# Kernel tuning notes

Hardware: AMD Instinct MI355X
Metric: run time of the kernel (lower is better)

The kernel has to match this reference:

```python
import jax, jax.numpy as jnp
import numpy as np

N, S, K, D, H = 65536, 5, 4, 12, 48  # batch, sq_len, max_node_num, nodefeat_n1, lstm hidden


def setup_inputs() -> dict:
    key = jax.random.key(0)
    ks = jax.random.split(key, 32)
    f = lambda i, shape, s=0.1: jax.random.normal(ks[i], shape, dtype=jnp.float32) * s
    return {
        'nodes_feature': f(0, (N, S, K, 6), 1.0),
        'pos': f(1, (N, S, K, 6), 1.0),
        'attmat': jax.random.uniform(ks[2], (N, S, K, K), dtype=jnp.float32),
        'msg_w': f(3, (D, D)), 'msg_b': f(4, (D,)),
        'gru_w_ih': f(5, (3 * D, D)), 'gru_w_hh': f(6, (3 * D, D)),
        'gru_b_ih': f(7, (3 * D,)), 'gru_b_hh': f(8, (3 * D,)),
        'lstm_w_ih_fw': f(9, (4 * H, H)), 'lstm_w_hh_fw': f(10, (4 * H, H)),
        'lstm_b_ih_fw': f(11, (4 * H,)), 'lstm_b_hh_fw': f(12, (4 * H,)),
        'lstm_w_ih_bw': f(13, (4 * H, H)), 'lstm_w_hh_bw': f(14, (4 * H, H)),
        'lstm_b_ih_bw': f(15, (4 * H,)), 'lstm_b_hh_bw': f(16, (4 * H,)),
        'en1_w': f(17, (H, 2 * H)), 'en1_b': f(18, (H,)),
        'en2_w': f(19, (36, H)), 'en2_b': f(20, (36,)),
        'en3_w': f(21, (6, 36)), 'en3_b': f(22, (6,)),
    }


def _gru_cell(x, h, w_ih, w_hh, b_ih, b_hh):
    # torch.nn.GRU single step: gates ordered r, z, n
    gi = x @ w_ih.T + b_ih
    gh = h @ w_hh.T + b_hh
    ir, iz, inn = jnp.split(gi, 3, axis=-1)
    hr, hz, hn = jnp.split(gh, 3, axis=-1)
    r = jax.nn.sigmoid(ir + hr)
    z = jax.nn.sigmoid(iz + hz)
    n = jnp.tanh(inn + r * hn)
    return (1.0 - z) * n + z * h


def _lstm_dir(x, w_ih, w_hh, b_ih, b_hh):
    # x: [T, N, H]; torch.nn.LSTM gates ordered i, f, g, o. Returns final hidden [N, H].
    nb = x.shape[1]
    hh = w_hh.shape[1]
    def step(carry, xt):
        h, c = carry
        g = xt @ w_ih.T + b_ih + h @ w_hh.T + b_hh
        i, fg, gg, o = jnp.split(g, 4, axis=-1)
        c = jax.nn.sigmoid(fg) * c + jax.nn.sigmoid(i) * jnp.tanh(gg)
        h = jax.nn.sigmoid(o) * jnp.tanh(c)
        return (h, c), None
    init = (jnp.zeros((nb, hh), x.dtype), jnp.zeros((nb, hh), x.dtype))
    (h, _), _ = jax.lax.scan(step, init, x)
    return h


def reference(nodes_feature, pos, attmat, msg_w, msg_b,
              gru_w_ih, gru_w_hh, gru_b_ih, gru_b_hh,
              lstm_w_ih_fw, lstm_w_hh_fw, lstm_b_ih_fw, lstm_b_hh_fw,
              lstm_w_ih_bw, lstm_w_hh_bw, lstm_b_ih_bw, lstm_b_hh_bw,
              en1_w, en1_b, en2_w, en2_b, en3_w, en3_b):
    node_feat = jnp.concatenate([nodes_feature, pos], axis=-1)  # [N,S,K,12]

    def message_pass(h):
        # message_fun on all neighbor states, attention-weighted sum, GRU update.
        m_all = h @ msg_w.T + msg_b                       # [N,S,K,12]
        m_v = jnp.einsum('bsnw,bswd->bsnd', attmat, m_all)  # [N,S,K,12]
        return _gru_cell(m_v, h, gru_w_ih, gru_w_hh, gru_b_ih, gru_b_hh)

    h = message_pass(node_feat)  # pass 0 (reads node_feat for h_v and h_w)
    h = message_pass(h)          # pass 1 (reads pass-0 hidden state)

    # hidden_node_state is stored [..., feat, node]; view(5,-1) flattens (feat, node)
    x = jnp.transpose(h, (0, 1, 3, 2)).reshape(h.shape[0], S, D * K)  # [N,S,48]
    xt = jnp.transpose(x, (1, 0, 2))  # [S,N,48]
    h_fw = _lstm_dir(xt, lstm_w_ih_fw, lstm_w_hh_fw, lstm_b_ih_fw, lstm_b_hh_fw)
    h_bw = _lstm_dir(xt[::-1], lstm_w_ih_bw, lstm_w_hh_bw, lstm_b_ih_bw, lstm_b_hh_bw)
    hn = jnp.concatenate([h_fw, h_bw], axis=-1)  # [N,96] == h_n.view(-1) per batch

    e = jax.nn.relu(hn @ en1_w.T + en1_b)
    e = jax.nn.relu(e @ en2_w.T + en2_b)
    return e @ en3_w.T + en3_b  # pred_label [N,6]
```

## Files before the change

kernel.cpp:

```cpp
#include <hip/hip_runtime.h>
#include <cstddef>

#define NB 65536
#define SL 5

typedef _Float16 f16;
typedef f16 half8 __attribute__((ext_vector_type(8)));
typedef float f32x4 __attribute__((ext_vector_type(4)));

__device__ __forceinline__ float sigm(float x) {
  return __builtin_amdgcn_rcpf(1.0f + __expf(-x));
}
__device__ __forceinline__ float tanh_f(float x) {
  return __builtin_fmaf(2.0f, __builtin_amdgcn_rcpf(1.0f + __expf(-2.0f * x)), -1.0f);
}
__device__ __forceinline__ unsigned int pkh2(float a, float b) {
  return (unsigned int)__builtin_bit_cast(unsigned short, (_Float16)a)
       | ((unsigned int)__builtin_bit_cast(unsigned short, (_Float16)b) << 16);
}
__device__ __forceinline__ unsigned int pku2(unsigned short a, unsigned short b) {
  return (unsigned int)a | ((unsigned int)b << 16);
}
__device__ __forceinline__ float loh(unsigned int u) {
  return (float)__builtin_bit_cast(_Float16, (unsigned short)(u & 0xffffu));
}
__device__ __forceinline__ float hih(unsigned int u) {
  return (float)__builtin_bit_cast(_Float16, (unsigned short)(u >> 16));
}

__global__ __launch_bounds__(256) void prep_kernel(
    const float* __restrict__ wi_fw, const float* __restrict__ wh_fw,
    const float* __restrict__ bi_fw, const float* __restrict__ bh_fw,
    const float* __restrict__ wi_bw, const float* __restrict__ wh_bw,
    const float* __restrict__ bi_bw, const float* __restrict__ bh_bw,
    const float* __restrict__ msg_w, const float* __restrict__ msg_b,
    const float* __restrict__ gw_ih, const float* __restrict__ gw_hh,
    const float* __restrict__ gb_ih, const float* __restrict__ gb_hh,
    unsigned short* __restrict__ wfrag, float* __restrict__ bsum,
    unsigned short* __restrict__ mfrag, float* __restrict__ mbias)
{
  const int t = blockIdx.x * 256 + threadIdx.x;
  if (t < 36864) {
    const int i = t & 7, lane = (t >> 3) & 63, fid = t >> 9;
    const int kc = fid % 3, mt = (fid / 3) % 3, ug = (fid / 9) & 3, dir = fid / 36;
    const int k = kc * 32 + (lane >> 4) * 8 + i;
    const int r16 = lane & 15;
    const int j = ug * 12 + mt * 4 + (r16 >> 2);
    const int g = r16 & 3;
    const float* wi = dir ? wi_bw : wi_fw;
    const float* wh = dir ? wh_bw : wh_fw;
    const float v = (k < 48) ? wi[(g * 48 + j) * 48 + k] : wh[(g * 48 + j) * 48 + (k - 48)];
    wfrag[t] = __builtin_bit_cast(unsigned short, (_Float16)v);
  } else if (t < 37248) {
    const int q = t - 36864;
    const int r16 = q & 15, mt = (q >> 4) % 3, ug = (q / 48) & 3, dir = q / 192;
    const int j = ug * 12 + mt * 4 + (r16 >> 2);
    const int g = r16 & 3;
    const int row = g * 48 + j;
    bsum[q] = dir ? (bi_bw[row] + bh_bw[row]) : (bi_fw[row] + bh_fw[row]);
  } else if (t < 39296) {
    const int q = t - 37248;
    const int i = q & 7, lane = (q >> 3) & 63, fid = q >> 9;
    const int k = ((lane >> 4) << 3) + i;
    const int r16 = lane & 15;
    float v = 0.0f;
    if (fid == 0) {
      if (r16 < 12 && k >= 12 && k < 24) v = msg_w[r16 * 12 + (k - 12)];
    } else {
      const int R = (fid - 1) * 16 + r16;
      const int kind = R / 12, j = R % 12;
      if (kind == 0)      v = (k < 12) ? gw_ih[j * 12 + k]          : ((k < 24) ? gw_hh[j * 12 + (k - 12)] : 0.0f);
      else if (kind == 1) v = (k < 12) ? gw_ih[(12 + j) * 12 + k]   : ((k < 24) ? gw_hh[(12 + j) * 12 + (k - 12)] : 0.0f);
      else if (kind == 2) v = (k < 12) ? gw_ih[(24 + j) * 12 + k]   : 0.0f;
      else                v = (k >= 12 && k < 24) ? gw_hh[(24 + j) * 12 + (k - 12)] : 0.0f;
    }
    mfrag[q] = __builtin_bit_cast(unsigned short, (_Float16)v);
  } else if (t < 39360) {
    const int q = t - 39296;
    if (q < 16) mbias[q] = (q < 12) ? msg_b[q] : 0.0f;
    else {
      const int R = q - 16, kind = R / 12, j = R % 12;
      float v;
      if (kind == 0)      v = gb_ih[j] + gb_hh[j];
      else if (kind == 1) v = gb_ih[12 + j] + gb_hh[12 + j];
      else if (kind == 2) v = gb_ih[24 + j];
      else                v = gb_hh[24 + j];
      mbias[q] = v;
    }
  }
}

__global__ __launch_bounds__(256) void msg_mfma_kernel(
    const float* __restrict__ nf, const float* __restrict__ pos,
    const float* __restrict__ att,
    const unsigned short* __restrict__ mfrag, const float* __restrict__ mbias,
    unsigned short* __restrict__ xth)
{
  __shared__ unsigned short B_lds[256][40];
  __shared__ unsigned short g_lds[256][50];
  unsigned short* xbuf = &g_lds[0][0];

  const int tid  = threadIdx.x;
  const int lane = tid & 63;
  const int w    = __builtin_amdgcn_readfirstlane(tid >> 6);
  const int c16  = lane & 15;
  const int grp  = lane >> 4;
  const int own  = tid;
  const int node = own & 3;
  const int sl   = (own >> 6) * 16 + ((own >> 4) & 3) * 4 + ((own >> 2) & 3);

  half8 A1 = *reinterpret_cast<const half8*>(mfrag + (size_t)lane * 8);
  half8 A2[3];
#pragma unroll
  for (int mt = 0; mt < 3; ++mt)
    A2[mt] = *reinterpret_cast<const half8*>(mfrag + (size_t)((1 + mt) * 64 + lane) * 8);
  const f32x4 bias1 = *reinterpret_cast<const f32x4*>(mbias + grp * 4);
  f32x4 bias2[3];
#pragma unroll
  for (int mt = 0; mt < 3; ++mt)
    bias2[mt] = *reinterpret_cast<const f32x4*>(mbias + 16 + mt * 16 + grp * 4);

  {
    unsigned int* bz = reinterpret_cast<unsigned int*>(&B_lds[0][0]);
#pragma unroll
    for (int q = 0; q < 6; ++q)  bz[tid * 20 + q] = 0u;
#pragma unroll
    for (int q = 12; q < 16; ++q) bz[tid * 20 + q] = 0u;
  }

  const int sid = blockIdx.x * 64 + sl;
  const int s   = sid >> 16;
  const int b   = sid & (NB - 1);
  float h[12];
  {
    const size_t ib = ((size_t)(b * SL + s) * 4 + node) * 6;
    const float2* n2 = (const float2*)(nf  + ib);
    const float2* p2 = (const float2*)(pos + ib);
#pragma unroll
    for (int q = 0; q < 3; q++) {
      float2 v = n2[q]; h[q*2]   = v.x; h[q*2+1]   = v.y;
      float2 u = p2[q]; h[6+q*2] = u.x; h[6+q*2+1] = u.y;
    }
  }
  float ta[4];
  {
    float4 v = *(const float4*)(att + ((size_t)(b * SL + s) * 4 + node) * 4);
    ta[0] = v.x; ta[1] = v.y; ta[2] = v.z; ta[3] = v.w;
  }
  {
    unsigned int* bp = (unsigned int*)&B_lds[own][0];
#pragma unroll
    for (int d = 0; d < 6; ++d) bp[6 + d] = pkh2(h[2*d], h[2*d+1]);
  }
  __syncthreads();

#pragma unroll 1
  for (int pass = 0; pass < 2; ++pass) {
#pragma unroll
    for (int nt = 0; nt < 4; ++nt) {
      const int col = w * 64 + nt * 16 + c16;
      half8 B = *reinterpret_cast<const half8*>(&B_lds[col][grp * 8]);
      f32x4 C = __builtin_amdgcn_mfma_f32_16x16x32_f16(A1, B, bias1, 0, 0, 0);
      if (grp < 3) {
        unsigned int* gp = (unsigned int*)&g_lds[col][0];
        gp[grp * 2]     = pkh2(C[0], C[1]);
        gp[grp * 2 + 1] = pkh2(C[2], C[3]);
      }
    }
    __syncthreads();

    {
      const int cb = own & ~3;
      float mv[12];
#pragma unroll
      for (int d = 0; d < 12; ++d) mv[d] = 0.0f;
#pragma unroll
      for (int ww = 0; ww < 4; ++ww) {
        const float a = ta[ww];
        const unsigned int* gp = (const unsigned int*)&g_lds[cb + ww][0];
#pragma unroll
        for (int dq = 0; dq < 6; ++dq) {
          const unsigned int u = gp[dq];
          mv[2*dq]   = __builtin_fmaf(a, loh(u), mv[2*dq]);
          mv[2*dq+1] = __builtin_fmaf(a, hih(u), mv[2*dq+1]);
        }
      }
      unsigned int* bp = (unsigned int*)&B_lds[own][0];
#pragma unroll
      for (int d = 0; d < 6; ++d) bp[d] = pkh2(mv[2*d], mv[2*d+1]);
    }
    __syncthreads();

#pragma unroll
    for (int nt = 0; nt < 4; ++nt) {
      const int col = w * 64 + nt * 16 + c16;
      half8 B = *reinterpret_cast<const half8*>(&B_lds[col][grp * 8]);
      f32x4 C0 = __builtin_amdgcn_mfma_f32_16x16x32_f16(A2[0], B, bias2[0], 0, 0, 0);
      f32x4 C1 = __builtin_amdgcn_mfma_f32_16x16x32_f16(A2[1], B, bias2[1], 0, 0, 0);
      f32x4 C2 = __builtin_amdgcn_mfma_f32_16x16x32_f16(A2[2], B, bias2[2], 0, 0, 0);
      unsigned int* gp = (unsigned int*)&g_lds[col][0];
      gp[grp * 2]      = pkh2(C0[0], C0[1]);
      gp[grp * 2 + 1]  = pkh2(C0[2], C0[3]);
      gp[8 + grp * 2]     = pkh2(C1[0], C1[1]);
      gp[8 + grp * 2 + 1] = pkh2(C1[2], C1[3]);
      gp[16 + grp * 2]     = pkh2(C2[0], C2[1]);
      gp[16 + grp * 2 + 1] = pkh2(C2[2], C2[3]);
    }
    __syncthreads();

    {
      unsigned int ur[6], uz[6], ui[6], uh[6];
      const unsigned int* gq = (const unsigned int*)&g_lds[own][0];
#pragma unroll
      for (int jq = 0; jq < 6; ++jq) {
        ur[jq] = gq[jq];
        uz[jq] = gq[6 + jq];
        ui[jq] = gq[12 + jq];
        uh[jq] = gq[18 + jq];
      }
      if (pass) __syncthreads();
#pragma unroll
      for (int jq = 0; jq < 6; ++jq) {
        {
          const float r = sigm(loh(ur[jq])), z = sigm(loh(uz[jq]));
          const float g = tanh_f(loh(ui[jq]) + r * loh(uh[jq]));
          h[2*jq] = (1.0f - z) * g + z * h[2*jq];
        }
        {
          const float r = sigm(hih(ur[jq])), z = sigm(hih(uz[jq]));
          const float g = tanh_f(hih(ui[jq]) + r * hih(uh[jq]));
          h[2*jq+1] = (1.0f - z) * g + z * h[2*jq+1];
        }
      }
      if (pass == 0) {
        unsigned int* bp = (unsigned int*)&B_lds[own][0];
#pragma unroll
        for (int d = 0; d < 6; ++d) bp[6 + d] = pkh2(h[2*d], h[2*d+1]);
      } else {
#pragma unroll
        for (int d = 0; d < 12; ++d)
          xbuf[sl * 50 + d * 4 + node] =
              __builtin_bit_cast(unsigned short, (_Float16)h[d]);
      }
    }
    __syncthreads();
  }

  const int b0   = (blockIdx.x * 64) & (NB - 1);
  const int sblk = blockIdx.x >> 10;
#pragma unroll
  for (int ff = 0; ff < 12; ++ff) {
    const int f = w * 12 + ff;
    xth[(size_t)(sblk * 48 + f) * NB + b0 + lane] = xbuf[lane * 50 + f];
  }
}

__global__ __launch_bounds__(512) void lstm_mfma_kernel(
    const unsigned short* __restrict__ xth,
    const unsigned short* __restrict__ wfrag,
    const float* __restrict__ bsum,
    const float* __restrict__ e1w, const float* __restrict__ e1b,
    const float* __restrict__ e2w, const float* __restrict__ e2b,
    const float* __restrict__ e3w, const float* __restrict__ e3b,
    float* __restrict__ out)
{
  __shared__ __align__(16) unsigned char poolc[33536];
  unsigned short* act = (unsigned short*)poolc;
  float*          hf  = (float*)poolc;
  unsigned short* e1o = (unsigned short*)(poolc + 26624);
  float*          e2o = (float*)poolc;

  const int tid  = threadIdx.x;
  const int lane = tid & 63;
  const int w    = __builtin_amdgcn_readfirstlane(tid >> 6);
  const int dir  = w & 1;
  const int ug   = w >> 1;
  const int b0   = blockIdx.x * 64;
  const int col  = lane & 15;
  const int grp  = lane >> 4;

  half8 A[3][3];
#pragma unroll
  for (int mt = 0; mt < 3; ++mt)
#pragma unroll
    for (int kc = 0; kc < 3; ++kc) {
      const int fid = ((dir * 4 + ug) * 3 + mt) * 3 + kc;
      A[mt][kc] = *reinterpret_cast<const half8*>(wfrag + (size_t)(fid * 64 + lane) * 8);
    }
  unsigned int bp[3][2];
#pragma unroll
  for (int mt = 0; mt < 3; ++mt) {
    const f32x4 bf = *reinterpret_cast<const f32x4*>(bsum + ((dir * 4 + ug) * 3 + mt) * 16 + grp * 4);
    bp[mt][0] = pkh2(bf[0], bf[1]);
    bp[mt][1] = pkh2(bf[2], bf[3]);
  }

  {
    unsigned short xa[6], xb[6];
#pragma unroll
    for (int ff = 0; ff < 6; ++ff) {
      const int f = w * 6 + ff;
      xa[ff] = xth[(size_t)(0 * 48 + f) * NB + b0 + lane];
      xb[ff] = xth[(size_t)(4 * 48 + f) * NB + b0 + lane];
    }
    unsigned int* a0 = (unsigned int*)&act[(0 * 64 + lane) * 104 + w * 6];
    unsigned int* a1 = (unsigned int*)&act[(1 * 64 + lane) * 104 + w * 6];
#pragma unroll
    for (int u = 0; u < 3; ++u) {
      a0[u] = pku2(xa[2*u], xa[2*u+1]);
      a1[u] = pku2(xb[2*u], xb[2*u+1]);
    }
  }
#pragma unroll
  for (int jj = 0; jj < 6; ++jj)
    *(unsigned int*)&act[(dir * 64 + lane) * 104 + 48 + ug * 12 + jj * 2] = 0u;
  __syncthreads();

  float c[3][4];
#pragma unroll
  for (int mt = 0; mt < 3; ++mt)
#pragma unroll
    for (int nt = 0; nt < 4; ++nt) c[mt][nt] = 0.0f;

#pragma unroll 1
  for (int st = 0; st < 5; ++st) {
    unsigned int hp[3][2];
#pragma unroll
    for (int nt = 0; nt < 4; ++nt) {
      const int n = nt * 16 + col;
      const unsigned short* ar = &act[(dir * 64 + n) * 104];
      half8 B0 = *reinterpret_cast<const half8*>(ar + grp * 8);
      half8 B1 = *reinterpret_cast<const half8*>(ar + 32 + grp * 8);
      half8 B2 = *reinterpret_cast<const half8*>(ar + 64 + grp * 8);
      f32x4 C0, C1, C2;
      C0[0] = loh(bp[0][0]); C0[1] = hih(bp[0][0]); C0[2] = loh(bp[0][1]); C0[3] = hih(bp[0][1]);
      C1[0] = loh(bp[1][0]); C1[1] = hih(bp[1][0]); C1[2] = loh(bp[1][1]); C1[3] = hih(bp[1][1]);
      C2[0] = loh(bp[2][0]); C2[1] = hih(bp[2][0]); C2[2] = loh(bp[2][1]); C2[3] = hih(bp[2][1]);
      C0 = __builtin_amdgcn_mfma_f32_16x16x32_f16(A[0][0], B0, C0, 0, 0, 0);
      C0 = __builtin_amdgcn_mfma_f32_16x16x32_f16(A[0][1], B1, C0, 0, 0, 0);
      C0 = __builtin_amdgcn_mfma_f32_16x16x32_f16(A[0][2], B2, C0, 0, 0, 0);
      C1 = __builtin_amdgcn_mfma_f32_16x16x32_f16(A[1][0], B0, C1, 0, 0, 0);
      C1 = __builtin_amdgcn_mfma_f32_16x16x32_f16(A[1][1], B1, C1, 0, 0, 0);
      C1 = __builtin_amdgcn_mfma_f32_16x16x32_f16(A[1][2], B2, C1, 0, 0, 0);
      C2 = __builtin_amdgcn_mfma_f32_16x16x32_f16(A[2][0], B0, C2, 0, 0, 0);
      C2 = __builtin_amdgcn_mfma_f32_16x16x32_f16(A[2][1], B1, C2, 0, 0, 0);
      C2 = __builtin_amdgcn_mfma_f32_16x16x32_f16(A[2][2], B2, C2, 0, 0, 0);
#pragma unroll
      for (int mt = 0; mt < 3; ++mt) {
        const f32x4 C = (mt == 0) ? C0 : (mt == 1) ? C1 : C2;
        const float cc = sigm(C[1]) * c[mt][nt] + sigm(C[0]) * tanh_f(C[2]);
        c[mt][nt] = cc;
        const float hv = sigm(C[3]) * tanh_f(cc);
        const unsigned short hb = __builtin_bit_cast(unsigned short, (_Float16)hv);
        if (nt & 1) hp[mt][nt >> 1] |= ((unsigned int)hb << 16);
        else        hp[mt][nt >> 1]  = (unsigned int)hb;
      }
    }
    __syncthreads();
    if (st < 4) {
#pragma unroll
      for (int mt = 0; mt < 3; ++mt)
#pragma unroll
        for (int nt = 0; nt < 4; ++nt)
          act[(dir * 64 + nt * 16 + col) * 104 + 48 + ug * 12 + mt * 4 + grp] =
              (unsigned short)(hp[mt][nt >> 1] >> (16 * (nt & 1)));
      const int s0 = st + 1, s1 = 3 - st;
      unsigned short xa[6], xb[6];
#pragma unroll
      for (int ff = 0; ff < 6; ++ff) {
        const int f = w * 6 + ff;
        xa[ff] = xth[(size_t)(s0 * 48 + f) * NB + b0 + lane];
        xb[ff] = xth[(size_t)(s1 * 48 + f) * NB + b0 + lane];
      }
      unsigned int* a0 = (unsigned int*)&act[(0 * 64 + lane) * 104 + w * 6];
      unsigned int* a1 = (unsigned int*)&act[(1 * 64 + lane) * 104 + w * 6];
#pragma unroll
      for (int u = 0; u < 3; ++u) {
        a0[u] = pku2(xa[2*u], xa[2*u+1]);
        a1[u] = pku2(xb[2*u], xb[2*u+1]);
      }
    } else {
#pragma unroll
      for (int mt = 0; mt < 3; ++mt)
#pragma unroll
        for (int nt = 0; nt < 4; ++nt)
          hf[(nt * 16 + col) * 100 + dir * 48 + ug * 12 + mt * 4 + grp] =
              (float)__builtin_bit_cast(_Float16,
                  (unsigned short)(hp[mt][nt >> 1] >> (16 * (nt & 1))));
    }
    __syncthreads();
  }

  {
    float acc[6];
#pragma unroll
    for (int r = 0; r < 6; ++r) acc[r] = e1b[w * 6 + r];
#pragma unroll
    for (int q = 0; q < 24; ++q) {
      const float4 v = *reinterpret_cast<const float4*>(&hf[lane * 100 + q * 4]);
#pragma unroll
      for (int r = 0; r < 6; ++r) {
        const int rr = w * 6 + r;
        acc[r] = __builtin_fmaf(e1w[rr * 96 + q * 4 + 0], v.x, acc[r]);
        acc[r] = __builtin_fmaf(e1w[rr * 96 + q * 4 + 1], v.y, acc[r]);
        acc[r] = __builtin_fmaf(e1w[rr * 96 + q * 4 + 2], v.z, acc[r]);
        acc[r] = __builtin_fmaf(e1w[rr * 96 + q * 4 + 3], v.w, acc[r]);
      }
    }
    __syncthreads();
    unsigned int* ep = (unsigned int*)&e1o[lane * 54];
#pragma unroll
    for (int u = 0; u < 3; ++u) {
      const float a0 = acc[2*u]   > 0.0f ? acc[2*u]   : 0.0f;
      const float a1 = acc[2*u+1] > 0.0f ? acc[2*u+1] : 0.0f;
      ep[w * 3 + u] = pkh2(a0, a1);
    }
  }
  __syncthreads();

  {
    const int e2base = (w < 4) ? w * 5 : 20 + (w - 4) * 4;
    const int e2cnt  = (w < 4) ? 5 : 4;
    float acc[5];
#pragma unroll
    for (int r = 0; r < 5; ++r) acc[r] = (r < e2cnt) ? e2b[e2base + r] : 0.0f;
    const unsigned int* eq = (const unsigned int*)&e1o[lane * 54];
#pragma unroll
    for (int q = 0; q < 24; ++q) {
      const unsigned int u = eq[q];
      const float v0 = loh(u), v1 = hih(u);
#pragma unroll
      for (int r = 0; r < 5; ++r) {
        if (r < e2cnt) {
          const int rr = e2base + r;
          acc[r] = __builtin_fmaf(e2w[rr * 48 + 2*q],     v0, acc[r]);
          acc[r] = __builtin_fmaf(e2w[rr * 48 + 2*q + 1], v1, acc[r]);
        }
      }
    }
    __syncthreads();
#pragma unroll
    for (int r = 0; r < 5; ++r)
      if (r < e2cnt) e2o[lane * 44 + e2base + r] = acc[r] > 0.0f ? acc[r] : 0.0f;
  }
  __syncthreads();

  if (w < 6) {
    float a = e3b[w];
#pragma unroll
    for (int q = 0; q < 9; ++q) {
      const float4 v = *reinterpret_cast<const float4*>(&e2o[lane * 44 + q * 4]);
      a = __builtin_fmaf(e3w[w * 36 + q * 4 + 0], v.x, a);
      a = __builtin_fmaf(e3w[w * 36 + q * 4 + 1], v.y, a);
      a = __builtin_fmaf(e3w[w * 36 + q * 4 + 2], v.z, a);
      a = __builtin_fmaf(e3w[w * 36 + q * 4 + 3], v.w, a);
    }
    out[(size_t)(b0 + lane) * 6 + w] = a;
  }
}

extern "C" void kernel_launch(void* const* d_in, const int* in_sizes, int n_in,
                              void* d_out, int out_size, void* d_ws, size_t ws_size,
                              hipStream_t stream)
{
  const float* nf    = (const float*)d_in[0];
  const float* pos   = (const float*)d_in[1];
  const float* att   = (const float*)d_in[2];
  const float* msg_w = (const float*)d_in[3];
  const float* msg_b = (const float*)d_in[4];
  const float* gw_ih = (const float*)d_in[5];
  const float* gw_hh = (const float*)d_in[6];
  const float* gb_ih = (const float*)d_in[7];
  const float* gb_hh = (const float*)d_in[8];
  const float* wi_fw = (const float*)d_in[9];
  const float* wh_fw = (const float*)d_in[10];
  const float* bi_fw = (const float*)d_in[11];
  const float* bh_fw = (const float*)d_in[12];
  const float* wi_bw = (const float*)d_in[13];
  const float* wh_bw = (const float*)d_in[14];
  const float* bi_bw = (const float*)d_in[15];
  const float* bh_bw = (const float*)d_in[16];
  const float* e1w   = (const float*)d_in[17];
  const float* e1b   = (const float*)d_in[18];
  const float* e2w   = (const float*)d_in[19];
  const float* e2b   = (const float*)d_in[20];
  const float* e3w   = (const float*)d_in[21];
  const float* e3b   = (const float*)d_in[22];

  unsigned short* xth   = (unsigned short*)d_ws;
  unsigned short* wfrag = xth + (size_t)SL * 48 * NB;
  float*          bsum  = (float*)(wfrag + 36864);
  unsigned short* mfrag = (unsigned short*)(bsum + 384);
  float*          mbias = (float*)(mfrag + 2048);
  float*          outp  = (float*)d_out;

  prep_kernel<<<154, 256, 0, stream>>>(
      wi_fw, wh_fw, bi_fw, bh_fw, wi_bw, wh_bw, bi_bw, bh_bw,
      msg_w, msg_b, gw_ih, gw_hh, gb_ih, gb_hh,
      wfrag, bsum, mfrag, mbias);

  msg_mfma_kernel<<<(NB * SL) / 64, 256, 0, stream>>>(
      nf, pos, att, mfrag, mbias, xth);

  lstm_mfma_kernel<<<NB / 64, 512, 0, stream>>>(
      xth, wfrag, bsum, e1w, e1b, e2w, e2b, e3w, e3b, outp);
}
```

Before: 132.1 us.

## Double-buffer LSTM hidden state in LDS to drop one barrier per step

The LSTM MFMA kernel now preloads x features 0..31 for all five timesteps into a separate LDS array. The hidden-state/x-tail buffer is ping-ponged between two halves, so each recurrent step needs one __syncthreads instead of two. Only the four trailing x features per step are fetched from global inside the loop. In exchange, LDS use per block roughly doubles (about 62 KB), which may reduce occupancy, and the MFMA B operand layout and padding change.

```diff
diff --git a/kernel.cpp b/kernel.cpp
--- a/kernel.cpp
+++ b/kernel.cpp
@@ -264,11 +264,12 @@
     const float* __restrict__ e3w, const float* __restrict__ e3b,
     float* __restrict__ out)
 {
-  __shared__ __align__(16) unsigned char poolc[33536];
-  unsigned short* act = (unsigned short*)poolc;
-  float*          hf  = (float*)poolc;
-  unsigned short* e1o = (unsigned short*)(poolc + 26624);
-  float*          e2o = (float*)poolc;
+  __shared__ __align__(16) unsigned char poolc[63744];
+  unsigned short* hb  = (unsigned short*)poolc;
+  unsigned short* xs  = (unsigned short*)(poolc + 36864);
+  float*          hf  = (float*)(poolc + 36864);
+  unsigned short* e1o = (unsigned short*)poolc;
+  float*          e2o = (float*)(poolc + 36864);
 
   const int tid  = threadIdx.x;
   const int lane = tid & 63;
@@ -296,24 +297,28 @@
   }
 
   {
-    unsigned short xa[6], xb[6];
-#pragma unroll
-    for (int ff = 0; ff < 6; ++ff) {
-      const int f = w * 6 + ff;
-      xa[ff] = xth[(size_t)(0 * 48 + f) * NB + b0 + lane];
-      xb[ff] = xth[(size_t)(4 * 48 + f) * NB + b0 + lane];
-    }
-    unsigned int* a0 = (unsigned int*)&act[(0 * 64 + lane) * 104 + w * 6];
-    unsigned int* a1 = (unsigned int*)&act[(1 * 64 + lane) * 104 + w * 6];
-#pragma unroll
-    for (int u = 0; u < 3; ++u) {
-      a0[u] = pku2(xa[2*u], xa[2*u+1]);
-      a1[u] = pku2(xb[2*u], xb[2*u+1]);
-    }
-  }
-#pragma unroll
-  for (int jj = 0; jj < 6; ++jj)
-    *(unsigned int*)&act[(dir * 64 + lane) * 104 + 48 + ug * 12 + jj * 2] = 0u;
+#pragma unroll
+    for (int s = 0; s < 5; ++s) {
+      unsigned short xa[4];
+#pragma unroll
+      for (int ff = 0; ff < 4; ++ff)
+        xa[ff] = xth[(size_t)(s * 48 + w * 4 + ff) * NB + b0 + lane];
+      unsigned int* xp = (unsigned int*)xs + (s * 64 + lane) * 21 + w * 2;
+      xp[0] = pku2(xa[0], xa[1]);
+      xp[1] = pku2(xa[2], xa[3]);
+    }
+    unsigned int* hz = (unsigned int*)hb + (dir * 64 + lane) * 36 + 8 + ug * 6;
+#pragma unroll
+    for (int jj = 0; jj < 6; ++jj) hz[jj] = 0u;
+    const int sp = dir ? 4 : 0;
+    unsigned short xv[4];
+#pragma unroll
+    for (int i = 0; i < 4; ++i)
+      xv[i] = xth[(size_t)(sp * 48 + 32 + ug * 4 + i) * NB + b0 + lane];
+    unsigned int* xc = (unsigned int*)hb + (dir * 64 + lane) * 36 + ug * 2;
+    xc[0] = pku2(xv[0], xv[1]);
+    xc[1] = pku2(xv[2], xv[3]);
+  }
   __syncthreads();
 
   float c[3][4];
@@ -324,14 +329,17 @@
 
 #pragma unroll 1
   for (int st = 0; st < 5; ++st) {
+    const int p  = st & 1;
+    const int s0 = dir ? (4 - st) : st;
+    const unsigned short* xrow = xs + (s0 * 64) * 42;
+    const unsigned short* hrow = hb + ((p * 2 + dir) * 64) * 72;
     unsigned int hp[3][2];
 #pragma unroll
     for (int nt = 0; nt < 4; ++nt) {
       const int n = nt * 16 + col;
-      const unsigned short* ar = &act[(dir * 64 + n) * 104];
-      half8 B0 = *reinterpret_cast<const half8*>(ar + grp * 8);
-      half8 B1 = *reinterpret_cast<const half8*>(ar + 32 + grp * 8);
-      half8 B2 = *reinterpret_cast<const half8*>(ar + 64 + grp * 8);
+      half8 B0 = *reinterpret_cast<const half8*>(xrow + n * 42 + grp * 8);
+      half8 B1 = *reinterpret_cast<const half8*>(hrow + n * 72 + grp * 8);
+      half8 B2 = *reinterpret_cast<const half8*>(hrow + n * 72 + 32 + grp * 8);
       f32x4 C0, C1, C2;
       C0[0] = loh(bp[0][0]); C0[1] = hih(bp[0][0]); C0[2] = loh(bp[0][1]); C0[3] = hih(bp[0][1]);
       C1[0] = loh(bp[1][0]); C1[1] = hih(bp[1][0]); C1[2] = loh(bp[1][1]); C1[3] = hih(bp[1][1]);
@@ -351,35 +359,30 @@
         const float cc = sigm(C[1]) * c[mt][nt] + sigm(C[0]) * tanh_f(C[2]);
         c[mt][nt] = cc;
         const float hv = sigm(C[3]) * tanh_f(cc);
-        const unsigned short hb = __builtin_bit_cast(unsigned short, (_Float16)hv);
-        if (nt & 1) hp[mt][nt >> 1] |= ((unsigned int)hb << 16);
-        else        hp[mt][nt >> 1]  = (unsigned int)hb;
-      }
-    }
-    __syncthreads();
+        const unsigned short hbb = __builtin_bit_cast(unsigned short, (_Float16)hv);
+        if (nt & 1) hp[mt][nt >> 1] |= ((unsigned int)hbb << 16);
+        else        hp[mt][nt >> 1]  = (unsigned int)hbb;
+      }
+    }
     if (st < 4) {
+      const int wb = ((1 - p) * 2 + dir) * 64;
 #pragma unroll
       for (int mt = 0; mt < 3; ++mt)
 #pragma unroll
         for (int nt = 0; nt < 4; ++nt)
-          act[(dir * 64 + nt * 16 + col) * 104 + 48 + ug * 12 + mt * 4 + grp] =
+          hb[(wb + nt * 16 + col) * 72 + 16 + ug * 12 + mt * 4 + grp] =
               (unsigned short)(hp[mt][nt >> 1] >> (16 * (nt & 1)));
-      const int s0 = st + 1, s1 = 3 - st;
-      unsigned short xa[6], xb[6];
-#pragma unroll
-      for (int ff = 0; ff < 6; ++ff) {
-        const int f = w * 6 + ff;
-        xa[ff] = xth[(size_t)(s0 * 48 + f) * NB + b0 + lane];
-        xb[ff] = xth[(size_t)(s1 * 48 + f) * NB + b0 + lane];
-      }
-      unsigned int* a0 = (unsigned int*)&act[(0 * 64 + lane) * 104 + w * 6];
-      unsigned int* a1 = (unsigned int*)&act[(1 * 64 + lane) * 104 + w * 6];
-#pragma unroll
-      for (int u = 0; u < 3; ++u) {
-        a0[u] = pku2(xa[2*u], xa[2*u+1]);
-        a1[u] = pku2(xb[2*u], xb[2*u+1]);
-      }
+      const int sp = dir ? (3 - st) : (st + 1);
+      unsigned short xv[4];
+#pragma unroll
+      for (int i = 0; i < 4; ++i)
+        xv[i] = xth[(size_t)(sp * 48 + 32 + ug * 4 + i) * NB + b0 + lane];
+      unsigned int* xc = (unsigned int*)hb + (wb + lane) * 36 + ug * 2;
+      xc[0] = pku2(xv[0], xv[1]);
+      xc[1] = pku2(xv[2], xv[3]);
+      __syncthreads();
     } else {
+      __syncthreads();
 #pragma unroll
       for (int mt = 0; mt < 3; ++mt)
 #pragma unroll
@@ -387,8 +390,8 @@
           hf[(nt * 16 + col) * 100 + dir * 48 + ug * 12 + mt * 4 + grp] =
               (float)__builtin_bit_cast(_Float16,
                   (unsigned short)(hp[mt][nt >> 1] >> (16 * (nt & 1))));
-    }
-    __syncthreads();
+      __syncthreads();
+    }
   }
 
   {
```

New measurement: 135.7 us. 2.8% more time.
